# Optimization experiments

Hardware: AMD Instinct MI355X
Metric: run time of the kernel (lower is better)

## Reference

```python
import jax, jax.numpy as jnp
import numpy as np

N_NODES = 100000
N_EDGES = 3200000
F_IN, F_HID, F_OUT = 512, 128, 32


def setup_inputs() -> dict:
    key = jax.random.key(0)
    ks = jax.random.split(key, 8)
    x = jax.random.normal(ks[0], (N_NODES, F_IN), dtype=jnp.float32)
    edge_row = jax.random.randint(ks[1], (N_EDGES,), 0, N_NODES, dtype=jnp.int32)
    edge_col = jax.random.randint(ks[2], (N_EDGES,), 0, N_NODES, dtype=jnp.int32)
    edge_val = jax.random.uniform(ks[3], (N_EDGES,), dtype=jnp.float32)
    W1 = jax.random.normal(ks[4], (F_IN, F_HID), dtype=jnp.float32) / np.sqrt(F_IN)
    b1 = jnp.zeros((F_HID,), dtype=jnp.float32)
    W2 = jax.random.normal(ks[5], (F_HID, F_OUT), dtype=jnp.float32) / np.sqrt(F_HID)
    b2 = jnp.zeros((F_OUT,), dtype=jnp.float32)
    return {"x": x, "edge_row": edge_row, "edge_col": edge_col,
            "edge_val": edge_val, "W1": W1, "b1": b1, "W2": W2, "b2": b2}


def _spmm(edge_row, edge_col, edge_val, dense):
    # out[r] = sum_{e: row[e]==r} val[e] * dense[col[e]]  (COO SpMM)
    gathered = dense[edge_col] * edge_val[:, None]  # [E, F]
    return jax.ops.segment_sum(gathered, edge_row, num_segments=N_NODES)


def reference(x, edge_row, edge_col, edge_val, W1, b1, W2, b2):
    # GraphConvolution 1: support = x@W1; out = A @ support + b1
    h = _spmm(edge_row, edge_col, edge_val, x @ W1) + b1
    h = jax.nn.relu(h)
    # GraphConvolution 2
    logits = _spmm(edge_row, edge_col, edge_val, h @ W2) + b2
    return jax.nn.log_softmax(logits, axis=1)
```

## Files before the change

### kernel.cpp

```cpp
#include <hip/hip_runtime.h>


#define NN 100000
#define NE 3200000
#define FIN 512
#define FHID 128
#define FOUT 32
#define BROWS 64
#define NBUCK 1563
#define NPART 256
#define CHUNK 12500
#define TOT (NBUCK * NPART)
#define NSCAN1 391
#define EBCAP 2560
#define EPT 25

typedef __attribute__((ext_vector_type(8))) short bf16x8;
typedef __attribute__((ext_vector_type(4))) float f32x4;

static __device__ __forceinline__ unsigned short f2bf(float f) {
    unsigned u = __float_as_uint(f);
    unsigned r = (u + 0x7FFFu + ((u >> 16) & 1u)) >> 16;
    return (unsigned short)r;
}
static __device__ __forceinline__ float bf2f(unsigned short u) {
    return __uint_as_float(((unsigned)u) << 16);
}
static __device__ __forceinline__ float bflo(unsigned u) {
    return __uint_as_float(u << 16);
}
static __device__ __forceinline__ float bfhi(unsigned u) {
    return __uint_as_float(u & 0xffff0000u);
}
static __device__ __forceinline__ bf16x8 pack8(float4 u, float4 v) {
    bf16x8 r;
    r[0] = (short)f2bf(u.x); r[1] = (short)f2bf(u.y);
    r[2] = (short)f2bf(u.z); r[3] = (short)f2bf(u.w);
    r[4] = (short)f2bf(v.x); r[5] = (short)f2bf(v.y);
    r[6] = (short)f2bf(v.z); r[7] = (short)f2bf(v.w);
    return r;
}

__global__ __launch_bounds__(256) void fused_prep_hist(const float* __restrict__ W1,
                                                       unsigned short* __restrict__ W1t,
                                                       const int* __restrict__ erow,
                                                       int* __restrict__ cntG) {
    if (blockIdx.x < NPART) {
        __shared__ int c[NBUCK];
        const int t = threadIdx.x;
        const int w = blockIdx.x;
        for (int i = t; i < NBUCK; i += 256) c[i] = 0;
        __syncthreads();
        const int e0 = w * CHUNK;
        const int e1 = min(e0 + CHUNK, NE);
        for (int e = e0 + t; e < e1; e += 256) atomicAdd(&c[erow[e] >> 6], 1);
        __syncthreads();
        for (int i = t; i < NBUCK; i += 256) cntG[w * NBUCK + i] = c[i];
    } else {
        int t = (blockIdx.x - NPART) * 256 + threadIdx.x;
        int j = t & 7;
        int c = t >> 3;
        int l = c & 63;
        int ks = (c >> 6) & 15;
        int nt = c >> 10;
        int n = nt * 16 + (l & 15);
        int k = ks * 32 + ((l >> 4) << 3) + j;
        W1t[(size_t)c * 8 + j] = f2bf(W1[k * FHID + n]);
    }
}

__global__ __launch_bounds__(256) void scan1_kernel(const int* __restrict__ cntG,
                                                    int* __restrict__ off,
                                                    int* __restrict__ partials) {
    __shared__ int s[256];
    int t = threadIdx.x;
    int i0 = blockIdx.x * 1024 + t * 4;
    int v[4];
#pragma unroll
    for (int j = 0; j < 4; ++j) {
        int i = i0 + j;
        v[j] = (i < TOT) ? cntG[(i & (NPART - 1)) * NBUCK + (i >> 8)] : 0;
    }
    int lsum = v[0] + v[1] + v[2] + v[3];
    s[t] = lsum;
    __syncthreads();
    for (int o = 1; o < 256; o <<= 1) {
        int xv = (t >= o) ? s[t - o] : 0;
        __syncthreads();
        s[t] += xv;
        __syncthreads();
    }
    if (t == 255) partials[blockIdx.x] = s[255];
    int run = s[t] - lsum;
#pragma unroll
    for (int j = 0; j < 4; ++j) {
        if (i0 + j < TOT) off[i0 + j] = run;
        run += v[j];
    }
}

__global__ __launch_bounds__(512) void scan2_kernel(int* partials) {
    __shared__ int s[512];
    int t = threadIdx.x;
    int v = (t < NSCAN1) ? partials[t] : 0;
    s[t] = v;
    __syncthreads();
    for (int o = 1; o < 512; o <<= 1) {
        int xv = (t >= o) ? s[t - o] : 0;
        __syncthreads();
        s[t] += xv;
        __syncthreads();
    }
    if (t < NSCAN1) partials[t] = s[t] - v;
}

__global__ __launch_bounds__(256) void scan3_kernel(int* __restrict__ off,
                                                    const int* __restrict__ partials) {
    int add = partials[blockIdx.x];
    int i0 = blockIdx.x * 1024 + threadIdx.x * 4;
#pragma unroll
    for (int j = 0; j < 4; ++j)
        if (i0 + j < TOT) off[i0 + j] += add;
}

__global__ __launch_bounds__(512) void scatter_part(const int* __restrict__ erow,
                                                    const int* __restrict__ ecol,
                                                    const float* __restrict__ eval,
                                                    const int* __restrict__ off,
                                                    int2* __restrict__ bcolval) {
    __shared__ int2 eb2[CHUNK];
    __shared__ unsigned short bkt2[CHUNK];
    __shared__ int cnt[NBUCK];
    __shared__ int pos[NBUCK];
    __shared__ int s[512];
    const int t = threadIdx.x;
    const int w = blockIdx.x;
    const int e0 = w * CHUNK;

    for (int i = t; i < NBUCK; i += 512) cnt[i] = 0;
    __syncthreads();

    int myb[EPT];
    int2 myrec[EPT];
#pragma unroll
    for (int ii = 0; ii < EPT; ++ii) {
        int i = t + ii * 512;
        myb[ii] = -1;
        if (i < CHUNK) {
            int e = e0 + i;
            int r = erow[e];
            int b = r >> 6;
            myb[ii] = b;
            myrec[ii] = make_int2(ecol[e] | ((r & 63) << 20), __float_as_int(eval[e]));
            atomicAdd(&cnt[b], 1);
        }
    }
    __syncthreads();

    int base = t * 4;
    int v[4];
#pragma unroll
    for (int j = 0; j < 4; ++j) v[j] = (base + j < NBUCK) ? cnt[base + j] : 0;
    int lsum = v[0] + v[1] + v[2] + v[3];
    s[t] = lsum;
    __syncthreads();
    for (int o = 1; o < 512; o <<= 1) {
        int xv = (t >= o) ? s[t - o] : 0;
        __syncthreads();
        s[t] += xv;
        __syncthreads();
    }
    int run = s[t] - lsum;
#pragma unroll
    for (int j = 0; j < 4; ++j) {
        if (base + j < NBUCK) cnt[base + j] = run;
        run += v[j];
    }
    __syncthreads();
    for (int i = t; i < NBUCK; i += 512) pos[i] = cnt[i];
    __syncthreads();

#pragma unroll
    for (int ii = 0; ii < EPT; ++ii) {
        if (myb[ii] >= 0) {
            int ld = atomicAdd(&pos[myb[ii]], 1);
            eb2[ld] = myrec[ii];
            bkt2[ld] = (unsigned short)myb[ii];
        }
    }
    __syncthreads();

    for (int i = t; i < CHUNK; i += 512) {
        int2 rec = eb2[i];
        int b = bkt2[i];
        int dest = off[b * NPART + w] + (i - cnt[b]);
        bcolval[dest] = rec;
    }
}

__global__ __launch_bounds__(256) void bucket_to_csr(const int* __restrict__ off,
                                                     const int2* __restrict__ bcolval,
                                                     int* __restrict__ rowptr,
                                                     int2* __restrict__ epack) {
    __shared__ int cnt[BROWS];
    __shared__ int pos[BROWS];
    __shared__ int s[BROWS];
    __shared__ int2 eb[EBCAP];
    const int b = blockIdx.x;
    const int t = threadIdx.x;
    const int s0 = off[b * NPART];
    const int send = (b == NBUCK - 1) ? NE : off[(b + 1) * NPART];
    const int n = send - s0;
    const bool fits = (n <= EBCAP);
    if (t < BROWS) cnt[t] = 0;
    __syncthreads();
    int2 myv[10];
    if (fits) {
#pragma unroll
        for (int ii = 0; ii < 10; ++ii) {
            int i = t + ii * 256;
            int2 v = make_int2(0, 0);
            if (i < n) {
                v = bcolval[s0 + i];
                atomicAdd(&cnt[((unsigned)v.x) >> 20], 1);
            }
            myv[ii] = v;
        }
    } else {
        for (int i = t; i < n; i += 256)
            atomicAdd(&cnt[((unsigned)bcolval[s0 + i].x) >> 20], 1);
    }
    __syncthreads();
    int myc = (t < BROWS) ? cnt[t] : 0;
    if (t < BROWS) s[t] = myc;
    __syncthreads();
    for (int o = 1; o < BROWS; o <<= 1) {
        int xv = (t >= o && t < BROWS) ? s[t - o] : 0;
        __syncthreads();
        if (t < BROWS) s[t] += xv;
        __syncthreads();
    }
    if (t < BROWS) {
        int excl = s[t] - myc;
        pos[t] = excl;
        int row = b * BROWS + t;
        if (row < NN) rowptr[row] = s0 + excl;
    }
    if (b == 0 && t == 0) rowptr[NN] = NE;
    __syncthreads();
    if (fits) {
#pragma unroll
        for (int ii = 0; ii < 10; ++ii) {
            int i = t + ii * 256;
            if (i < n) {
                int2 v = myv[ii];
                int p = atomicAdd(&pos[((unsigned)v.x) >> 20], 1);
                eb[p] = make_int2(v.x & 0xFFFFF, v.y);
            }
        }
        __syncthreads();
        for (int i = t; i < n; i += 256) epack[s0 + i] = eb[i];
    } else {
        for (int i = t; i < n; i += 256) {
            int2 v = bcolval[s0 + i];
            int p = atomicAdd(&pos[((unsigned)v.x) >> 20], 1);
            epack[s0 + p] = make_int2(v.x & 0xFFFFF, v.y);
        }
    }
}

__global__ __launch_bounds__(256) void gemm1_mfma(const float* __restrict__ x,
                                                  const unsigned short* __restrict__ W1t,
                                                  unsigned short* __restrict__ out) {
    const int tid = threadIdx.x;
    const int lane = tid & 63;
    const int w = tid >> 6;
    const int quad = lane >> 4;
    const int m = lane & 15;
    const int row0 = blockIdx.x * 128 + w * 32;

    int rA = row0 + m;
    int rB = row0 + 16 + m;
    rA = rA < NN ? rA : NN - 1;
    rB = rB < NN ? rB : NN - 1;
    const float* pA = x + (size_t)rA * FIN + quad * 8;
    const float* pB = x + (size_t)rB * FIN + quad * 8;

    f32x4 acc[2][8];
#pragma unroll
    for (int i = 0; i < 2; ++i)
#pragma unroll
        for (int nt = 0; nt < 8; ++nt) acc[i][nt] = (f32x4){0.f, 0.f, 0.f, 0.f};

    float4 a0 = *(const float4*)pA;
    float4 a1 = *(const float4*)(pA + 4);
    float4 b0 = *(const float4*)pB;
    float4 b1 = *(const float4*)(pB + 4);

    for (int ks = 0; ks < 16; ++ks) {
        const int kn = (ks + 1) & 15;
        float4 na0 = *(const float4*)(pA + kn * 32);
        float4 na1 = *(const float4*)(pA + kn * 32 + 4);
        float4 nb0 = *(const float4*)(pB + kn * 32);
        float4 nb1 = *(const float4*)(pB + kn * 32 + 4);

        bf16x8 fA = pack8(a0, a1);
        bf16x8 fB = pack8(b0, b1);
        bf16x8 bb[8];
#pragma unroll
        for (int nt = 0; nt < 8; ++nt)
            bb[nt] = *(const bf16x8*)(W1t + ((size_t)((nt * 16 + ks) * 64 + lane)) * 8);
#pragma unroll
        for (int nt = 0; nt < 8; ++nt) {
            acc[0][nt] = __builtin_amdgcn_mfma_f32_16x16x32_bf16(fA, bb[nt], acc[0][nt], 0, 0, 0);
            acc[1][nt] = __builtin_amdgcn_mfma_f32_16x16x32_bf16(fB, bb[nt], acc[1][nt], 0, 0, 0);
        }
        a0 = na0; a1 = na1; b0 = nb0; b1 = nb1;
    }

#pragma unroll
    for (int i = 0; i < 2; ++i)
#pragma unroll
        for (int nt = 0; nt < 8; ++nt) {
            int col = nt * 16 + m;
#pragma unroll
            for (int r = 0; r < 4; ++r) {
                int row = row0 + i * 16 + quad * 4 + r;
                if (row < NN) out[(size_t)row * FHID + col] = f2bf(acc[i][nt][r]);
            }
        }
}

__global__ __launch_bounds__(256) void spmm1_kernel(const int* __restrict__ rowptr,
                                                    const int2* __restrict__ epack,
                                                    const unsigned short* __restrict__ dense,
                                                    const float* __restrict__ b1,
                                                    unsigned short* __restrict__ h) {
    const int lane = threadIdx.x & 63;
    const int row = blockIdx.x * 4 + (threadIdx.x >> 6);
    const int start = __builtin_amdgcn_readfirstlane(rowptr[row]);
    const int cnt = __builtin_amdgcn_readfirstlane(rowptr[row + 1]) - start;
    const int sl16 = lane & 15;
    const unsigned* d32 = (const unsigned*)dense;
    float acc0 = 0.f, acc1 = 0.f;

    int j = 0;
    for (; j + 32 <= cnt; j += 32) {
        int2 p0 = epack[start + j + sl16];
        int2 p1 = epack[start + j + 16 + sl16];
        unsigned d[32];
#pragma unroll
        for (int k = 0; k < 16; ++k) {
            int c = __builtin_amdgcn_readlane(p0.x, k);
            d[k] = d32[((size_t)c << 6) + lane];
        }
#pragma unroll
        for (int k = 0; k < 16; ++k) {
            int c = __builtin_amdgcn_readlane(p1.x, k);
            d[16 + k] = d32[((size_t)c << 6) + lane];
        }
#pragma unroll
        for (int k = 0; k < 16; ++k) {
            float v = __int_as_float(__builtin_amdgcn_readlane(p0.y, k));
            acc0 = fmaf(v, bflo(d[k]), acc0);
            acc1 = fmaf(v, bfhi(d[k]), acc1);
        }
#pragma unroll
        for (int k = 0; k < 16; ++k) {
            float v = __int_as_float(__builtin_amdgcn_readlane(p1.y, k));
            acc0 = fmaf(v, bflo(d[16 + k]), acc0);
            acc1 = fmaf(v, bfhi(d[16 + k]), acc1);
        }
    }
    if (j + 16 <= cnt) {
        int2 p = epack[start + j + sl16];
        unsigned d[16];
#pragma unroll
        for (int k = 0; k < 16; ++k) {
            int c = __builtin_amdgcn_readlane(p.x, k);
            d[k] = d32[((size_t)c << 6) + lane];
        }
#pragma unroll
        for (int k = 0; k < 16; ++k) {
            float v = __int_as_float(__builtin_amdgcn_readlane(p.y, k));
            acc0 = fmaf(v, bflo(d[k]), acc0);
            acc1 = fmaf(v, bfhi(d[k]), acc1);
        }
        j += 16;
    }
    const int rem = cnt - j;
    if (rem > 0) {
        int idx = j + (sl16 < rem ? sl16 : rem - 1);
        int2 p = epack[start + idx];
        unsigned d[16];
#pragma unroll
        for (int k = 0; k < 16; ++k) {
            int c = __builtin_amdgcn_readlane(p.x, k);
            c = (k < rem) ? c : 0;
            d[k] = d32[((size_t)c << 6) + lane];
        }
#pragma unroll
        for (int k = 0; k < 16; ++k) {
            float v = (k < rem) ? __int_as_float(__builtin_amdgcn_readlane(p.y, k)) : 0.f;
            acc0 = fmaf(v, bflo(d[k]), acc0);
            acc1 = fmaf(v, bfhi(d[k]), acc1);
        }
    }
    float2 bb = *(const float2*)(b1 + lane * 2);
    unsigned r0 = f2bf(fmaxf(acc0 + bb.x, 0.f));
    unsigned r1 = f2bf(fmaxf(acc1 + bb.y, 0.f));
    *((unsigned*)(h + (size_t)row * FHID) + lane) = r0 | (r1 << 16);
}

__global__ __launch_bounds__(256) void gemm2_kernel(const unsigned short* __restrict__ h,
                                                    const float* __restrict__ W2,
                                                    unsigned short* __restrict__ out) {
    __shared__ float hs[64][129];
    const int tid = threadIdx.x;
    const int lane = tid & 63;
    const int cg = __builtin_amdgcn_readfirstlane(tid >> 6);
    const int row0 = blockIdx.x * 64;
    const int row = row0 + lane;

    float acc[8];
#pragma unroll
    for (int c = 0; c < 8; ++c) acc[c] = 0.f;

#pragma unroll
    for (int j = 0; j < 8; ++j) {
        int f4 = tid + j * 256;
        int r = f4 >> 5;
        int kq = f4 & 31;
        ushort4 v = make_ushort4(0, 0, 0, 0);
        if (row0 + r < NN) v = *(const ushort4*)(h + (size_t)(row0 + r) * FHID + kq * 4);
        hs[r][kq * 4 + 0] = bf2f(v.x);
        hs[r][kq * 4 + 1] = bf2f(v.y);
        hs[r][kq * 4 + 2] = bf2f(v.z);
        hs[r][kq * 4 + 3] = bf2f(v.w);
    }
    __syncthreads();
#pragma unroll 4
    for (int k = 0; k < FHID; ++k) {
        float a = hs[lane][k];
        const float* wrow = W2 + k * FOUT + cg * 8;
#pragma unroll
        for (int c = 0; c < 8; ++c) acc[c] += a * wrow[c];
    }
    if (row < NN) {
        uint4 st;
        st.x = (unsigned)f2bf(acc[0]) | ((unsigned)f2bf(acc[1]) << 16);
        st.y = (unsigned)f2bf(acc[2]) | ((unsigned)f2bf(acc[3]) << 16);
        st.z = (unsigned)f2bf(acc[4]) | ((unsigned)f2bf(acc[5]) << 16);
        st.w = (unsigned)f2bf(acc[6]) | ((unsigned)f2bf(acc[7]) << 16);
        *(uint4*)(out + (size_t)row * FOUT + cg * 8) = st;
    }
}

__global__ __launch_bounds__(256) void spmm2_kernel(const int* __restrict__ rowptr,
                                                    const int2* __restrict__ epack,
                                                    const unsigned short* __restrict__ dense,
                                                    const float* __restrict__ b2,
                                                    float* __restrict__ out) {
    const int lane = threadIdx.x & 63;
    const int row = blockIdx.x * 4 + (threadIdx.x >> 6);
    const int start = __builtin_amdgcn_readfirstlane(rowptr[row]);
    const int cnt = __builtin_amdgcn_readfirstlane(rowptr[row + 1]) - start;
    const int quad = lane >> 4;
    const int sl16 = lane & 15;
    const unsigned* d32 = (const unsigned*)dense;
    float acc0 = 0.f, acc1 = 0.f;

    int j = 0;
    for (; j + 16 <= cnt; j += 16) {
        int2 p = epack[start + j + sl16];
        unsigned d[4];
        float vv[4];
#pragma unroll
        for (int k = 0; k < 16; ++k) {
            int c = __builtin_amdgcn_readlane(p.x, k);
            int v = __builtin_amdgcn_readlane(p.y, k);
            if ((k >> 2) == quad) {
                d[k & 3] = d32[((size_t)c << 4) + sl16];
                vv[k & 3] = __int_as_float(v);
            }
        }
#pragma unroll
        for (int k = 0; k < 4; ++k) {
            acc0 = fmaf(vv[k], bflo(d[k]), acc0);
            acc1 = fmaf(vv[k], bfhi(d[k]), acc1);
        }
    }
    const int rem = cnt - j;
    if (rem > 0) {
        int idx = j + (sl16 < rem ? sl16 : rem - 1);
        int2 p = epack[start + idx];
        unsigned d[4];
        float vv[4];
#pragma unroll
        for (int k = 0; k < 4; ++k) { d[k] = 0; vv[k] = 0.f; }
#pragma unroll
        for (int k = 0; k < 16; ++k) {
            int c = __builtin_amdgcn_readlane(p.x, k);
            int v = __builtin_amdgcn_readlane(p.y, k);
            c = (k < rem) ? c : 0;
            if ((k >> 2) == quad) {
                d[k & 3] = d32[((size_t)c << 4) + sl16];
                vv[k & 3] = (k < rem) ? __int_as_float(v) : 0.f;
            }
        }
#pragma unroll
        for (int k = 0; k < 4; ++k) {
            acc0 = fmaf(vv[k], bflo(d[k]), acc0);
            acc1 = fmaf(vv[k], bfhi(d[k]), acc1);
        }
    }
    acc0 += __shfl_xor(acc0, 16, 64);
    acc0 += __shfl_xor(acc0, 32, 64);
    acc1 += __shfl_xor(acc1, 16, 64);
    acc1 += __shfl_xor(acc1, 32, 64);
    float2 bb = *(const float2*)(b2 + sl16 * 2);
    acc0 += bb.x;
    acc1 += bb.y;
    float m = fmaxf(acc0, acc1);
#pragma unroll
    for (int mask = 8; mask >= 1; mask >>= 1) m = fmaxf(m, __shfl_xor(m, mask, 64));
    float ssum = expf(acc0 - m) + expf(acc1 - m);
#pragma unroll
    for (int mask = 8; mask >= 1; mask >>= 1) ssum += __shfl_xor(ssum, mask, 64);
    float lse = m + logf(ssum);
    if (lane < 16) {
        float2 st = make_float2(acc0 - lse, acc1 - lse);
        *(float2*)(out + (size_t)row * FOUT + sl16 * 2) = st;
    }
}

extern "C" void kernel_launch(void* const* d_in, const int* in_sizes, int n_in,
                              void* d_out, int out_size, void* d_ws, size_t ws_size,
                              hipStream_t stream) {
    const float* x = (const float*)d_in[0];
    const int* erow = (const int*)d_in[1];
    const int* ecol = (const int*)d_in[2];
    const float* eval = (const float*)d_in[3];
    const float* W1 = (const float*)d_in[4];
    const float* b1 = (const float*)d_in[5];
    const float* W2 = (const float*)d_in[6];
    const float* b2 = (const float*)d_in[7];
    float* out = (float*)d_out;

    char* ws = (char*)d_ws;
    size_t off_b = 0;
    auto walloc = [&](size_t bytes) -> void* {
        void* p = ws + off_b;
        off_b = (off_b + bytes + 255) & ~(size_t)255;
        return p;
    };
    int2* epack = (int2*)walloc((size_t)NE * 8);
    int* rowptr = (int*)walloc((size_t)(NN + 1) * 4);
    int* cntG = (int*)walloc((size_t)TOT * 4);
    int* off = (int*)walloc((size_t)TOT * 4);
    int* partials = (int*)walloc(4096);
    unsigned short* W1t = (unsigned short*)walloc((size_t)FHID * FIN * 2);
    int2* bcolval = (int2*)walloc((size_t)NE * 8);
    unsigned short* support1 = (unsigned short*)walloc((size_t)NN * FHID * 2);
    unsigned short* h = (unsigned short*)walloc((size_t)NN * FHID * 2);
    unsigned short* support2 = support1;

    fused_prep_hist<<<NPART + 256, 256, 0, stream>>>(W1, W1t, erow, cntG);
    scan1_kernel<<<NSCAN1, 256, 0, stream>>>(cntG, off, partials);
    scan2_kernel<<<1, 512, 0, stream>>>(partials);
    scan3_kernel<<<NSCAN1, 256, 0, stream>>>(off, partials);
    scatter_part<<<NPART, 512, 0, stream>>>(erow, ecol, eval, off, bcolval);
    bucket_to_csr<<<NBUCK, 256, 0, stream>>>(off, bcolval, rowptr, epack);
    gemm1_mfma<<<(NN + 127) / 128, 256, 0, stream>>>(x, W1t, support1);
    spmm1_kernel<<<NN / 4, 256, 0, stream>>>(rowptr, epack, support1, b1, h);
    gemm2_kernel<<<(NN + 63) / 64, 256, 0, stream>>>(h, W2, support2);
    spmm2_kernel<<<NN / 4, 256, 0, stream>>>(rowptr, epack, support2, b2, out);
}
```

Before: 606.4 us.

## Fuse scan fixup, CSR build with GEMM1, and GEMM2 into SpMM1

Drops the scan3 pass. scatter_part and the CSR builder now add the block partials themselves when they read offsets. The bucket-to-CSR kernel and the GEMM1 MFMA kernel run as one launch, with block ranges split between the two independent jobs so they can overlap. GEMM2 is folded into a persistent SpMM1 kernel that keeps W2 in LDS and multiplies each h row through cross-lane readlane, so h is never written to global memory. The costs are extra per-row serial work (64 readlanes per row) and a fixed grid of 2048 blocks for SpMM1.

```diff
diff --git a/kernel.cpp b/kernel.cpp
--- a/kernel.cpp
+++ b/kernel.cpp
@@ -14,6 +14,7 @@
 #define NSCAN1 391
 #define EBCAP 2560
 #define EPT 25
+#define GG1 ((NN + 127) / 128)
 
 typedef __attribute__((ext_vector_type(8))) short bf16x8;
 typedef __attribute__((ext_vector_type(4))) float f32x4;
@@ -114,24 +115,17 @@
     if (t < NSCAN1) partials[t] = s[t] - v;
 }
 
-__global__ __launch_bounds__(256) void scan3_kernel(int* __restrict__ off,
-                                                    const int* __restrict__ partials) {
-    int add = partials[blockIdx.x];
-    int i0 = blockIdx.x * 1024 + threadIdx.x * 4;
-#pragma unroll
-    for (int j = 0; j < 4; ++j)
-        if (i0 + j < TOT) off[i0 + j] += add;
-}
-
 __global__ __launch_bounds__(512) void scatter_part(const int* __restrict__ erow,
                                                     const int* __restrict__ ecol,
                                                     const float* __restrict__ eval,
                                                     const int* __restrict__ off,
+                                                    const int* __restrict__ partials,
                                                     int2* __restrict__ bcolval) {
     __shared__ int2 eb2[CHUNK];
     __shared__ unsigned short bkt2[CHUNK];
     __shared__ int cnt[NBUCK];
     __shared__ int pos[NBUCK];
+    __shared__ int ofsG[NBUCK];
     __shared__ int s[512];
     const int t = threadIdx.x;
     const int w = blockIdx.x;
@@ -177,7 +171,11 @@
         run += v[j];
     }
     __syncthreads();
-    for (int i = t; i < NBUCK; i += 512) pos[i] = cnt[i];
+    for (int i = t; i < NBUCK; i += 512) {
+        pos[i] = cnt[i];
+        int fi = i * NPART + w;
+        ofsG[i] = off[fi] + partials[fi >> 10];
+    }
     __syncthreads();
 
 #pragma unroll
@@ -193,266 +191,245 @@
     for (int i = t; i < CHUNK; i += 512) {
         int2 rec = eb2[i];
         int b = bkt2[i];
-        int dest = off[b * NPART + w] + (i - cnt[b]);
+        int dest = ofsG[b] + (i - cnt[b]);
         bcolval[dest] = rec;
     }
 }
 
-__global__ __launch_bounds__(256) void bucket_to_csr(const int* __restrict__ off,
-                                                     const int2* __restrict__ bcolval,
-                                                     int* __restrict__ rowptr,
-                                                     int2* __restrict__ epack) {
+__global__ __launch_bounds__(256) void fused_csr_gemm1(
+    const int* __restrict__ off, const int* __restrict__ partials,
+    const int2* __restrict__ bcolval, int* __restrict__ rowptr,
+    int2* __restrict__ epack,
+    const float* __restrict__ x, const unsigned short* __restrict__ W1t,
+    unsigned short* __restrict__ outd) {
     __shared__ int cnt[BROWS];
     __shared__ int pos[BROWS];
     __shared__ int s[BROWS];
     __shared__ int2 eb[EBCAP];
-    const int b = blockIdx.x;
+    if (blockIdx.x < NBUCK) {
+        const int b = blockIdx.x;
+        const int t = threadIdx.x;
+        const int fi = b * NPART;
+        const int s0 = off[fi] + partials[fi >> 10];
+        const int send = (b == NBUCK - 1)
+                             ? NE
+                             : off[fi + NPART] + partials[(fi + NPART) >> 10];
+        const int n = send - s0;
+        const bool fits = (n <= EBCAP);
+        if (t < BROWS) cnt[t] = 0;
+        __syncthreads();
+        int2 myv[10];
+        if (fits) {
+#pragma unroll
+            for (int ii = 0; ii < 10; ++ii) {
+                int i = t + ii * 256;
+                int2 v = make_int2(0, 0);
+                if (i < n) {
+                    v = bcolval[s0 + i];
+                    atomicAdd(&cnt[((unsigned)v.x) >> 20], 1);
+                }
+                myv[ii] = v;
+            }
+        } else {
+            for (int i = t; i < n; i += 256)
+                atomicAdd(&cnt[((unsigned)bcolval[s0 + i].x) >> 20], 1);
+        }
+        __syncthreads();
+        int myc = (t < BROWS) ? cnt[t] : 0;
+        if (t < BROWS) s[t] = myc;
+        __syncthreads();
+        for (int o = 1; o < BROWS; o <<= 1) {
+            int xv = (t >= o && t < BROWS) ? s[t - o] : 0;
+            __syncthreads();
+            if (t < BROWS) s[t] += xv;
+            __syncthreads();
+        }
+        if (t < BROWS) {
+            int excl = s[t] - myc;
+            pos[t] = excl;
+            int row = b * BROWS + t;
+            if (row < NN) rowptr[row] = s0 + excl;
+        }
+        if (b == 0 && t == 0) rowptr[NN] = NE;
+        __syncthreads();
+        if (fits) {
+#pragma unroll
+            for (int ii = 0; ii < 10; ++ii) {
+                int i = t + ii * 256;
+                if (i < n) {
+                    int2 v = myv[ii];
+                    int p = atomicAdd(&pos[((unsigned)v.x) >> 20], 1);
+                    eb[p] = make_int2(v.x & 0xFFFFF, v.y);
+                }
+            }
+            __syncthreads();
+            for (int i = t; i < n; i += 256) epack[s0 + i] = eb[i];
+        } else {
+            for (int i = t; i < n; i += 256) {
+                int2 v = bcolval[s0 + i];
+                int p = atomicAdd(&pos[((unsigned)v.x) >> 20], 1);
+                epack[s0 + p] = make_int2(v.x & 0xFFFFF, v.y);
+            }
+        }
+    } else {
+        const int tid = threadIdx.x;
+        const int lane = tid & 63;
+        const int w = tid >> 6;
+        const int quad = lane >> 4;
+        const int m = lane & 15;
+        const int row0 = (blockIdx.x - NBUCK) * 128 + w * 32;
+
+        int rA = row0 + m;
+        int rB = row0 + 16 + m;
+        rA = rA < NN ? rA : NN - 1;
+        rB = rB < NN ? rB : NN - 1;
+        const float* pA = x + (size_t)rA * FIN + quad * 8;
+        const float* pB = x + (size_t)rB * FIN + quad * 8;
+
+        f32x4 acc[2][8];
+#pragma unroll
+        for (int i = 0; i < 2; ++i)
+#pragma unroll
+            for (int nt = 0; nt < 8; ++nt) acc[i][nt] = (f32x4){0.f, 0.f, 0.f, 0.f};
+
+        float4 a0 = *(const float4*)pA;
+        float4 a1 = *(const float4*)(pA + 4);
+        float4 b0 = *(const float4*)pB;
+        float4 b1 = *(const float4*)(pB + 4);
+
+        for (int ks = 0; ks < 16; ++ks) {
+            const int kn = (ks + 1) & 15;
+            float4 na0 = *(const float4*)(pA + kn * 32);
+            float4 na1 = *(const float4*)(pA + kn * 32 + 4);
+            float4 nb0 = *(const float4*)(pB + kn * 32);
+            float4 nb1 = *(const float4*)(pB + kn * 32 + 4);
+
+            bf16x8 fA = pack8(a0, a1);
+            bf16x8 fB = pack8(b0, b1);
+            bf16x8 bb[8];
+#pragma unroll
+            for (int nt = 0; nt < 8; ++nt)
+                bb[nt] = *(const bf16x8*)(W1t + ((size_t)((nt * 16 + ks) * 64 + lane)) * 8);
+#pragma unroll
+            for (int nt = 0; nt < 8; ++nt) {
+                acc[0][nt] = __builtin_amdgcn_mfma_f32_16x16x32_bf16(fA, bb[nt], acc[0][nt], 0, 0, 0);
+                acc[1][nt] = __builtin_amdgcn_mfma_f32_16x16x32_bf16(fB, bb[nt], acc[1][nt], 0, 0, 0);
+            }
+            a0 = na0; a1 = na1; b0 = nb0; b1 = nb1;
+        }
+
+#pragma unroll
+        for (int i = 0; i < 2; ++i)
+#pragma unroll
+            for (int nt = 0; nt < 8; ++nt) {
+                int col = nt * 16 + m;
+#pragma unroll
+                for (int r = 0; r < 4; ++r) {
+                    int row = row0 + i * 16 + quad * 4 + r;
+                    if (row < NN) outd[(size_t)row * FHID + col] = f2bf(acc[i][nt][r]);
+                }
+            }
+    }
+}
+
+__global__ __launch_bounds__(256) void spmm1_fused(const int* __restrict__ rowptr,
+                                                   const int2* __restrict__ epack,
+                                                   const unsigned short* __restrict__ dense,
+                                                   const float* __restrict__ b1,
+                                                   const float* __restrict__ W2,
+                                                   unsigned short* __restrict__ support2) {
+    __shared__ float w2l[FHID * FOUT];
     const int t = threadIdx.x;
-    const int s0 = off[b * NPART];
-    const int send = (b == NBUCK - 1) ? NE : off[(b + 1) * NPART];
-    const int n = send - s0;
-    const bool fits = (n <= EBCAP);
-    if (t < BROWS) cnt[t] = 0;
-    __syncthreads();
-    int2 myv[10];
-    if (fits) {
-#pragma unroll
-        for (int ii = 0; ii < 10; ++ii) {
-            int i = t + ii * 256;
-            int2 v = make_int2(0, 0);
-            if (i < n) {
-                v = bcolval[s0 + i];
-                atomicAdd(&cnt[((unsigned)v.x) >> 20], 1);
-            }
-            myv[ii] = v;
-        }
-    } else {
-        for (int i = t; i < n; i += 256)
-            atomicAdd(&cnt[((unsigned)bcolval[s0 + i].x) >> 20], 1);
-    }
-    __syncthreads();
-    int myc = (t < BROWS) ? cnt[t] : 0;
-    if (t < BROWS) s[t] = myc;
-    __syncthreads();
-    for (int o = 1; o < BROWS; o <<= 1) {
-        int xv = (t >= o && t < BROWS) ? s[t - o] : 0;
-        __syncthreads();
-        if (t < BROWS) s[t] += xv;
-        __syncthreads();
-    }
-    if (t < BROWS) {
-        int excl = s[t] - myc;
-        pos[t] = excl;
-        int row = b * BROWS + t;
-        if (row < NN) rowptr[row] = s0 + excl;
-    }
-    if (b == 0 && t == 0) rowptr[NN] = NE;
-    __syncthreads();
-    if (fits) {
-#pragma unroll
-        for (int ii = 0; ii < 10; ++ii) {
-            int i = t + ii * 256;
-            if (i < n) {
-                int2 v = myv[ii];
-                int p = atomicAdd(&pos[((unsigned)v.x) >> 20], 1);
-                eb[p] = make_int2(v.x & 0xFFFFF, v.y);
-            }
-        }
-        __syncthreads();
-        for (int i = t; i < n; i += 256) epack[s0 + i] = eb[i];
-    } else {
-        for (int i = t; i < n; i += 256) {
-            int2 v = bcolval[s0 + i];
-            int p = atomicAdd(&pos[((unsigned)v.x) >> 20], 1);
-            epack[s0 + p] = make_int2(v.x & 0xFFFFF, v.y);
-        }
-    }
-}
-
-__global__ __launch_bounds__(256) void gemm1_mfma(const float* __restrict__ x,
-                                                  const unsigned short* __restrict__ W1t,
-                                                  unsigned short* __restrict__ out) {
-    const int tid = threadIdx.x;
-    const int lane = tid & 63;
-    const int w = tid >> 6;
-    const int quad = lane >> 4;
-    const int m = lane & 15;
-    const int row0 = blockIdx.x * 128 + w * 32;
-
-    int rA = row0 + m;
-    int rB = row0 + 16 + m;
-    rA = rA < NN ? rA : NN - 1;
-    rB = rB < NN ? rB : NN - 1;
-    const float* pA = x + (size_t)rA * FIN + quad * 8;
-    const float* pB = x + (size_t)rB * FIN + quad * 8;
-
-    f32x4 acc[2][8];
-#pragma unroll
-    for (int i = 0; i < 2; ++i)
-#pragma unroll
-        for (int nt = 0; nt < 8; ++nt) acc[i][nt] = (f32x4){0.f, 0.f, 0.f, 0.f};
-
-    float4 a0 = *(const float4*)pA;
-    float4 a1 = *(const float4*)(pA + 4);
-    float4 b0 = *(const float4*)pB;
-    float4 b1 = *(const float4*)(pB + 4);
-
-    for (int ks = 0; ks < 16; ++ks) {
-        const int kn = (ks + 1) & 15;
-        float4 na0 = *(const float4*)(pA + kn * 32);
-        float4 na1 = *(const float4*)(pA + kn * 32 + 4);
-        float4 nb0 = *(const float4*)(pB + kn * 32);
-        float4 nb1 = *(const float4*)(pB + kn * 32 + 4);
-
-        bf16x8 fA = pack8(a0, a1);
-        bf16x8 fB = pack8(b0, b1);
-        bf16x8 bb[8];
-#pragma unroll
-        for (int nt = 0; nt < 8; ++nt)
-            bb[nt] = *(const bf16x8*)(W1t + ((size_t)((nt * 16 + ks) * 64 + lane)) * 8);
-#pragma unroll
-        for (int nt = 0; nt < 8; ++nt) {
-            acc[0][nt] = __builtin_amdgcn_mfma_f32_16x16x32_bf16(fA, bb[nt], acc[0][nt], 0, 0, 0);
-            acc[1][nt] = __builtin_amdgcn_mfma_f32_16x16x32_bf16(fB, bb[nt], acc[1][nt], 0, 0, 0);
-        }
-        a0 = na0; a1 = na1; b0 = nb0; b1 = nb1;
-    }
-
-#pragma unroll
-    for (int i = 0; i < 2; ++i)
-#pragma unroll
-        for (int nt = 0; nt < 8; ++nt) {
-            int col = nt * 16 + m;
-#pragma unroll
-            for (int r = 0; r < 4; ++r) {
-                int row = row0 + i * 16 + quad * 4 + r;
-                if (row < NN) out[(size_t)row * FHID + col] = f2bf(acc[i][nt][r]);
-            }
-        }
-}
-
-__global__ __launch_bounds__(256) void spmm1_kernel(const int* __restrict__ rowptr,
-                                                    const int2* __restrict__ epack,
-                                                    const unsigned short* __restrict__ dense,
-                                                    const float* __restrict__ b1,
-                                                    unsigned short* __restrict__ h) {
-    const int lane = threadIdx.x & 63;
-    const int row = blockIdx.x * 4 + (threadIdx.x >> 6);
-    const int start = __builtin_amdgcn_readfirstlane(rowptr[row]);
-    const int cnt = __builtin_amdgcn_readfirstlane(rowptr[row + 1]) - start;
+#pragma unroll
+    for (int i = 0; i < 16; ++i) w2l[t + i * 256] = W2[t + i * 256];
+    __syncthreads();
+
+    const int lane = t & 63;
     const int sl16 = lane & 15;
+    const int sfts = (lane >> 5) ? 0 : 16;
     const unsigned* d32 = (const unsigned*)dense;
-    float acc0 = 0.f, acc1 = 0.f;
-
-    int j = 0;
-    for (; j + 32 <= cnt; j += 32) {
-        int2 p0 = epack[start + j + sl16];
-        int2 p1 = epack[start + j + 16 + sl16];
-        unsigned d[32];
-#pragma unroll
-        for (int k = 0; k < 16; ++k) {
-            int c = __builtin_amdgcn_readlane(p0.x, k);
-            d[k] = d32[((size_t)c << 6) + lane];
-        }
-#pragma unroll
-        for (int k = 0; k < 16; ++k) {
-            int c = __builtin_amdgcn_readlane(p1.x, k);
-            d[16 + k] = d32[((size_t)c << 6) + lane];
-        }
-#pragma unroll
-        for (int k = 0; k < 16; ++k) {
-            float v = __int_as_float(__builtin_amdgcn_readlane(p0.y, k));
-            acc0 = fmaf(v, bflo(d[k]), acc0);
-            acc1 = fmaf(v, bfhi(d[k]), acc1);
-        }
-#pragma unroll
-        for (int k = 0; k < 16; ++k) {
-            float v = __int_as_float(__builtin_amdgcn_readlane(p1.y, k));
-            acc0 = fmaf(v, bflo(d[16 + k]), acc0);
-            acc1 = fmaf(v, bfhi(d[16 + k]), acc1);
-        }
-    }
-    if (j + 16 <= cnt) {
-        int2 p = epack[start + j + sl16];
-        unsigned d[16];
-#pragma unroll
-        for (int k = 0; k < 16; ++k) {
-            int c = __builtin_amdgcn_readlane(p.x, k);
-            d[k] = d32[((size_t)c << 6) + lane];
-        }
-#pragma unroll
-        for (int k = 0; k < 16; ++k) {
-            float v = __int_as_float(__builtin_amdgcn_readlane(p.y, k));
-            acc0 = fmaf(v, bflo(d[k]), acc0);
-            acc1 = fmaf(v, bfhi(d[k]), acc1);
-        }
-        j += 16;
-    }
-    const int rem = cnt - j;
-    if (rem > 0) {
-        int idx = j + (sl16 < rem ? sl16 : rem - 1);
-        int2 p = epack[start + idx];
-        unsigned d[16];
-#pragma unroll
-        for (int k = 0; k < 16; ++k) {
-            int c = __builtin_amdgcn_readlane(p.x, k);
-            c = (k < rem) ? c : 0;
-            d[k] = d32[((size_t)c << 6) + lane];
-        }
-#pragma unroll
-        for (int k = 0; k < 16; ++k) {
-            float v = (k < rem) ? __int_as_float(__builtin_amdgcn_readlane(p.y, k)) : 0.f;
-            acc0 = fmaf(v, bflo(d[k]), acc0);
-            acc1 = fmaf(v, bfhi(d[k]), acc1);
-        }
-    }
-    float2 bb = *(const float2*)(b1 + lane * 2);
-    unsigned r0 = f2bf(fmaxf(acc0 + bb.x, 0.f));
-    unsigned r1 = f2bf(fmaxf(acc1 + bb.y, 0.f));
-    *((unsigned*)(h + (size_t)row * FHID) + lane) = r0 | (r1 << 16);
-}
-
-__global__ __launch_bounds__(256) void gemm2_kernel(const unsigned short* __restrict__ h,
-                                                    const float* __restrict__ W2,
-                                                    unsigned short* __restrict__ out) {
-    __shared__ float hs[64][129];
-    const int tid = threadIdx.x;
-    const int lane = tid & 63;
-    const int cg = __builtin_amdgcn_readfirstlane(tid >> 6);
-    const int row0 = blockIdx.x * 64;
-    const int row = row0 + lane;
-
-    float acc[8];
-#pragma unroll
-    for (int c = 0; c < 8; ++c) acc[c] = 0.f;
-
-#pragma unroll
-    for (int j = 0; j < 8; ++j) {
-        int f4 = tid + j * 256;
-        int r = f4 >> 5;
-        int kq = f4 & 31;
-        ushort4 v = make_ushort4(0, 0, 0, 0);
-        if (row0 + r < NN) v = *(const ushort4*)(h + (size_t)(row0 + r) * FHID + kq * 4);
-        hs[r][kq * 4 + 0] = bf2f(v.x);
-        hs[r][kq * 4 + 1] = bf2f(v.y);
-        hs[r][kq * 4 + 2] = bf2f(v.z);
-        hs[r][kq * 4 + 3] = bf2f(v.w);
-    }
-    __syncthreads();
-#pragma unroll 4
-    for (int k = 0; k < FHID; ++k) {
-        float a = hs[lane][k];
-        const float* wrow = W2 + k * FOUT + cg * 8;
-#pragma unroll
-        for (int c = 0; c < 8; ++c) acc[c] += a * wrow[c];
-    }
-    if (row < NN) {
-        uint4 st;
-        st.x = (unsigned)f2bf(acc[0]) | ((unsigned)f2bf(acc[1]) << 16);
-        st.y = (unsigned)f2bf(acc[2]) | ((unsigned)f2bf(acc[3]) << 16);
-        st.z = (unsigned)f2bf(acc[4]) | ((unsigned)f2bf(acc[5]) << 16);
-        st.w = (unsigned)f2bf(acc[6]) | ((unsigned)f2bf(acc[7]) << 16);
-        *(uint4*)(out + (size_t)row * FOUT + cg * 8) = st;
+    const float2 bb = *(const float2*)(b1 + lane * 2);
+    const int nwaves = gridDim.x * 4;
+
+    for (int row = blockIdx.x * 4 + (t >> 6); row < NN; row += nwaves) {
+        const int start = __builtin_amdgcn_readfirstlane(rowptr[row]);
+        const int cnt = __builtin_amdgcn_readfirstlane(rowptr[row + 1]) - start;
+        float acc0 = 0.f, acc1 = 0.f;
+
+        int j = 0;
+        for (; j + 32 <= cnt; j += 32) {
+            int2 p0 = epack[start + j + sl16];
+            int2 p1 = epack[start + j + 16 + sl16];
+            unsigned d[32];
+#pragma unroll
+            for (int k = 0; k < 16; ++k) {
+                int c = __builtin_amdgcn_readlane(p0.x, k);
+                d[k] = d32[((size_t)c << 6) + lane];
+            }
+#pragma unroll
+            for (int k = 0; k < 16; ++k) {
+                int c = __builtin_amdgcn_readlane(p1.x, k);
+                d[16 + k] = d32[((size_t)c << 6) + lane];
+            }
+#pragma unroll
+            for (int k = 0; k < 16; ++k) {
+                float v = __int_as_float(__builtin_amdgcn_readlane(p0.y, k));
+                acc0 = fmaf(v, bflo(d[k]), acc0);
+                acc1 = fmaf(v, bfhi(d[k]), acc1);
+            }
+#pragma unroll
+            for (int k = 0; k < 16; ++k) {
+                float v = __int_as_float(__builtin_amdgcn_readlane(p1.y, k));
+                acc0 = fmaf(v, bflo(d[16 + k]), acc0);
+                acc1 = fmaf(v, bfhi(d[16 + k]), acc1);
+            }
+        }
+        if (j + 16 <= cnt) {
+            int2 p = epack[start + j + sl16];
+            unsigned d[16];
+#pragma unroll
+            for (int k = 0; k < 16; ++k) {
+                int c = __builtin_amdgcn_readlane(p.x, k);
+                d[k] = d32[((size_t)c << 6) + lane];
+            }
+#pragma unroll
+            for (int k = 0; k < 16; ++k) {
+                float v = __int_as_float(__builtin_amdgcn_readlane(p.y, k));
+                acc0 = fmaf(v, bflo(d[k]), acc0);
+                acc1 = fmaf(v, bfhi(d[k]), acc1);
+            }
+            j += 16;
+        }
+        const int rem = cnt - j;
+        if (rem > 0) {
+            int idx = j + (sl16 < rem ? sl16 : rem - 1);
+            int2 p = epack[start + idx];
+            unsigned d[16];
+#pragma unroll
+            for (int k = 0; k < 16; ++k) {
+                int c = __builtin_amdgcn_readlane(p.x, k);
+                c = (k < rem) ? c : 0;
+                d[k] = d32[((size_t)c << 6) + lane];
+            }
+#pragma unroll
+            for (int k = 0; k < 16; ++k) {
+                float v = (k < rem) ? __int_as_float(__builtin_amdgcn_readlane(p.y, k)) : 0.f;
+                acc0 = fmaf(v, bflo(d[k]), acc0);
+                acc1 = fmaf(v, bfhi(d[k]), acc1);
+            }
+        }
+        float h0 = fmaxf(acc0 + bb.x, 0.f);
+        float h1 = fmaxf(acc1 + bb.y, 0.f);
+        unsigned packed = (unsigned)f2bf(h0) | ((unsigned)f2bf(h1) << 16);
+        float p = 0.f;
+#pragma unroll
+        for (int jj = 0; jj < 64; ++jj) {
+            unsigned pk = (unsigned)__builtin_amdgcn_readlane(packed, jj);
+            float hv = __uint_as_float((pk << sfts) & 0xffff0000u);
+            p = fmaf(hv, w2l[jj * 64 + lane], p);
+        }
+        p += __shfl_xor(p, 32, 64);
+        if (lane < 32) support2[(size_t)row * FOUT + lane] = f2bf(p);
     }
 }
 
@@ -562,17 +539,14 @@
     unsigned short* W1t = (unsigned short*)walloc((size_t)FHID * FIN * 2);
     int2* bcolval = (int2*)walloc((size_t)NE * 8);
     unsigned short* support1 = (unsigned short*)walloc((size_t)NN * FHID * 2);
-    unsigned short* h = (unsigned short*)walloc((size_t)NN * FHID * 2);
-    unsigned short* support2 = support1;
+    unsigned short* support2 = (unsigned short*)walloc((size_t)NN * FOUT * 2);
 
     fused_prep_hist<<<NPART + 256, 256, 0, stream>>>(W1, W1t, erow, cntG);
     scan1_kernel<<<NSCAN1, 256, 0, stream>>>(cntG, off, partials);
     scan2_kernel<<<1, 512, 0, stream>>>(partials);
-    scan3_kernel<<<NSCAN1, 256, 0, stream>>>(off, partials);
-    scatter_part<<<NPART, 512, 0, stream>>>(erow, ecol, eval, off, bcolval);
-    bucket_to_csr<<<NBUCK, 256, 0, stream>>>(off, bcolval, rowptr, epack);
-    gemm1_mfma<<<(NN + 127) / 128, 256, 0, stream>>>(x, W1t, support1);
-    spmm1_kernel<<<NN / 4, 256, 0, stream>>>(rowptr, epack, support1, b1, h);
-    gemm2_kernel<<<(NN + 63) / 64, 256, 0, stream>>>(h, W2, support2);
+    scatter_part<<<NPART, 512, 0, stream>>>(erow, ecol, eval, off, partials, bcolval);
+    fused_csr_gemm1<<<NBUCK + GG1, 256, 0, stream>>>(off, partials, bcolval, rowptr,
+                                                     epack, x, W1t, support1);
+    spmm1_fused<<<2048, 256, 0, stream>>>(rowptr, epack, support1, b1, W2, support2);
     spmm2_kernel<<<NN / 4, 256, 0, stream>>>(rowptr, epack, support2, b2, out);
 }
```

After: 596.7 us. About the same (-1.6%).
